# Kernel tuning notes

Measured on AMD Instinct MI355X. Metric: run time of the kernel, lower is better.

The kernel has to match this reference:

```python
import jax, jax.numpy as jnp
import numpy as np

THRESHOLDS = (0.3, 0.4, 0.5)
EPS_NORM = 1e-12   # F.normalize eps
EPS_MAX = 1e-5     # added to max before rescale


def setup_inputs() -> dict:
    key = jax.random.key(0)
    k1, k2 = jax.random.split(key)
    cam = jax.random.uniform(k1, (4, 64, 64), dtype=jnp.float32)
    feat = jax.random.normal(k2, (4, 256, 64, 64), dtype=jnp.float32)
    return {"cam": cam, "feat": feat}


def reference(cam, feat):
    # multi-threshold soft mask: mean of hard masks at each threshold -> (B,1,H,W)
    masks = jnp.stack([(cam >= t).astype(feat.dtype) for t in THRESHOLDS], axis=1)
    m = masks.mean(axis=1)[:, None]  # (B,1,H,W)
    masked = feat * m  # (B,C,H,W)

    B, C, H, W = masked.shape
    f = masked.reshape(B, C, H * W)  # (B,C,N)
    # L2-normalize over channel dim (torch F.normalize, dim=1)
    norm = jnp.sqrt(jnp.sum(f * f, axis=1, keepdims=True))
    fn = f / jnp.maximum(norm, EPS_NORM)

    # full pairwise similarity (B,N,N), then CAM-weighted aggregation
    sim = jnp.einsum('bcn,bcm->bnm', fn, fn)      # (B,N,N)
    camf = cam.reshape(B, H * W)                  # (B,N)
    out = jnp.einsum('bnm,bm->bn', sim, camf)     # (B,N)

    mn = out.min(axis=1, keepdims=True)
    mx = out.max(axis=1, keepdims=True) + EPS_MAX
    ref = ((out - mn) / (mx - mn)).reshape(B, H, W)

    loss = jnp.mean(jnp.abs(ref - jax.lax.stop_gradient(cam)))
    return ref, loss
```

## Files before the change

kernel.cpp:

```cpp
#include <hip/hip_runtime.h>


constexpr int B  = 4;
constexpr int C  = 256;
constexpr int N  = 4096;
constexpr int BN = B * N;
constexpr int CN = C * N;

__device__ __forceinline__ float wsum(float v) {
#pragma unroll
    for (int o = 32; o > 0; o >>= 1) v += __shfl_down(v, o, 64);
    return v;
}
__device__ __forceinline__ float wmin64(float v) {
#pragma unroll
    for (int o = 32; o > 0; o >>= 1) v = fminf(v, __shfl_down(v, o, 64));
    return v;
}
__device__ __forceinline__ float wmax64(float v) {
#pragma unroll
    for (int o = 32; o > 0; o >>= 1) v = fmaxf(v, __shfl_down(v, o, 64));
    return v;
}

__global__ void __launch_bounds__(256) k_norm(
    const float* __restrict__ cam, const float* __restrict__ feat,
    float* __restrict__ s, float* __restrict__ w, unsigned int* __restrict__ cnt)
{
    if (blockIdx.x == 0 && threadIdx.x == 0) *cnt = 0u;
    const int t   = threadIdx.x;
    const int pix = t & 31;
    const int g   = t >> 5;
    const int p   = blockIdx.x * 32 + pix;
    const int b   = p >> 12;
    const int n   = p & (N - 1);

    const float* fp = feat + (size_t)b * CN + (size_t)(g * 32) * N + n;
    float ss = 0.f;
#pragma unroll 8
    for (int cc = 0; cc < 32; ++cc) {
        float x = fp[(size_t)cc * N];
        ss = fmaf(x, x, ss);
    }
    __shared__ float red[8][33];
    red[g][pix] = ss;
    __syncthreads();
    if (t < 32) {
        float tot = 0.f;
#pragma unroll
        for (int gg = 0; gg < 8; ++gg) tot += red[gg][t];
        float cv = cam[blockIdx.x * 32 + t];
        float m  = ((cv >= 0.3f ? 1.f : 0.f) + (cv >= 0.4f ? 1.f : 0.f) +
                    (cv >= 0.5f ? 1.f : 0.f)) * (1.f / 3.f);
        tot *= m * m;
        float sc = m / fmaxf(sqrtf(tot), 1e-12f);
        int q = blockIdx.x * 32 + t;
        s[q] = sc;
        w[q] = sc * cv;
    }
}

__global__ void __launch_bounds__(256) k_v(
    const float* __restrict__ feat, const float* __restrict__ w,
    float* __restrict__ v)
{
    const int bc = blockIdx.x;
    const int b = bc >> 8, c = bc & (C - 1);
    const float* fp = feat + (size_t)b * CN + (size_t)c * N;
    const float* wp = w + b * N;
    const int t = threadIdx.x;
    float acc = 0.f;
#pragma unroll
    for (int i = 0; i < 4; ++i) {
        int idx = (i * 256 + t) * 4;
        float4 x = *(const float4*)(fp + idx);
        float4 y = *(const float4*)(wp + idx);
        acc = fmaf(x.x, y.x, acc); acc = fmaf(x.y, y.y, acc);
        acc = fmaf(x.z, y.z, acc); acc = fmaf(x.w, y.w, acc);
    }
    __shared__ float red[4];
    float tot = wsum(acc);
    if ((t & 63) == 0) red[t >> 6] = tot;
    __syncthreads();
    if (t == 0) v[bc] = (red[0] + red[1]) + (red[2] + red[3]);
}

__global__ void __launch_bounds__(256) k_out(
    const float* __restrict__ feat, const float* __restrict__ s,
    const float* __restrict__ v, float* __restrict__ ob,
    float* __restrict__ bmn, float* __restrict__ bmx)
{
    const int t   = threadIdx.x;
    const int pix = t & 31;
    const int g   = t >> 5;
    const int p   = blockIdx.x * 32 + pix;
    const int b   = p >> 12;
    const int n   = p & (N - 1);

    __shared__ float vs[C];
    vs[t] = v[b * C + t];
    __syncthreads();

    const float* fp = feat + (size_t)b * CN + (size_t)(g * 32) * N + n;
    float acc = 0.f;
#pragma unroll 8
    for (int cc = 0; cc < 32; ++cc)
        acc = fmaf(fp[(size_t)cc * N], vs[g * 32 + cc], acc);

    __shared__ float red[8][33];
    red[g][pix] = acc;
    __syncthreads();
    if (t < 32) {
        float tot = 0.f;
#pragma unroll
        for (int gg = 0; gg < 8; ++gg) tot += red[gg][t];
        float o = s[blockIdx.x * 32 + t] * tot;
        ob[blockIdx.x * 32 + t] = o;
        float mn = o, mx = o;
#pragma unroll
        for (int o2 = 16; o2 > 0; o2 >>= 1) {
            mn = fminf(mn, __shfl_down(mn, o2, 64));
            mx = fmaxf(mx, __shfl_down(mx, o2, 64));
        }
        if (t == 0) { bmn[blockIdx.x] = mn; bmx[blockIdx.x] = mx; }
    }
}

__global__ void __launch_bounds__(256) k_final(
    const float* __restrict__ ob, const float* __restrict__ cam,
    const float* __restrict__ bmn, const float* __restrict__ bmx,
    float* __restrict__ out, float* __restrict__ part, unsigned int* __restrict__ cnt)
{
    const int t = threadIdx.x, blk = blockIdx.x;
    const int p = blk * 256 + t;
    const int b = blk >> 4;

    __shared__ float sh[2];
    if (t < 64) {
        float a = fminf(bmn[b * 128 + t], bmn[b * 128 + 64 + t]);
        a = wmin64(a);
        if (t == 0) sh[0] = a;
    } else if (t < 128) {
        int l = t - 64;
        float a = fmaxf(bmx[b * 128 + l], bmx[b * 128 + 64 + l]);
        a = wmax64(a);
        if (l == 0) sh[1] = a;
    }
    __syncthreads();
    const float mn = sh[0];
    const float mx = sh[1] + 1e-5f;

    float r = (ob[p] - mn) / (mx - mn);
    out[p] = r;
    float ad = fabsf(r - cam[p]);

    __shared__ float red[4];
    float ps = wsum(ad);
    if ((t & 63) == 0) red[t >> 6] = ps;
    __syncthreads();

    __shared__ int lastflag;
    if (t == 0) {
        float tot = (red[0] + red[1]) + (red[2] + red[3]);
        __hip_atomic_store(&part[blk], tot, __ATOMIC_RELEASE, __HIP_MEMORY_SCOPE_AGENT);
        unsigned old = __hip_atomic_fetch_add(cnt, 1u, __ATOMIC_ACQ_REL,
                                              __HIP_MEMORY_SCOPE_AGENT);
        lastflag = (old == 63u) ? 1 : 0;
    }
    __syncthreads();
    if (lastflag && t < 64) {
        float x = __hip_atomic_load(&part[t], __ATOMIC_ACQUIRE,
                                    __HIP_MEMORY_SCOPE_AGENT);
        x = wsum(x);
        if (t == 0) out[BN] = x * (1.f / (float)BN);
    }
}

extern "C" void kernel_launch(void* const* d_in, const int* in_sizes, int n_in,
                              void* d_out, int out_size, void* d_ws, size_t ws_size,
                              hipStream_t stream) {
    const float* cam  = (const float*)d_in[0];
    const float* feat = (const float*)d_in[1];
    float* out = (float*)d_out;
    float* ws  = (float*)d_ws;

    float* s    = ws;
    float* w    = ws + 16384;
    float* v    = ws + 32768;
    float* ob   = ws + 33792;
    float* bmn  = ws + 50176;
    float* bmx  = ws + 50688;
    float* part = ws + 51200;
    unsigned int* cnt = (unsigned int*)(ws + 51264);

    k_norm <<<512,  256, 0, stream>>>(cam, feat, s, w, cnt);
    k_v    <<<1024, 256, 0, stream>>>(feat, w, v);
    k_out  <<<512,  256, 0, stream>>>(feat, s, v, ob, bmn, bmx);
    k_final<<<64,   256, 0, stream>>>(ob, cam, bmn, bmx, out, part, cnt);
}
```

Measured before the change: 20.37 us.

## Fuse channel-weighted reduction into norm kernel with partial sums and small reduce

Computes per-block partial sums of feat weighted by the normalized CAM weights inside the norm kernel, reusing the feature tile just loaded, instead of a separate kernel that re-reads all of feat. A small 4-block kernel then sums the 128 partials per batch into v. This removes one full pass over the feature tensor but adds a partial-sum buffer and a low-parallelism reduction kernel.

Measured after the change: 23.06 us. 13.2% more time.

```diff
diff --git a/kernel.cpp b/kernel.cpp
--- a/kernel.cpp
+++ b/kernel.cpp
@@ -6,6 +6,7 @@
 constexpr int N  = 4096;
 constexpr int BN = B * N;
 constexpr int CN = C * N;
+constexpr int NBLK1 = 512;
 
 __device__ __forceinline__ float wsum(float v) {
 #pragma unroll
@@ -23,66 +24,72 @@
     return v;
 }
 
-__global__ void __launch_bounds__(256) k_norm(
+__global__ void __launch_bounds__(256) k_norm_vpart(
     const float* __restrict__ cam, const float* __restrict__ feat,
-    float* __restrict__ s, float* __restrict__ w, unsigned int* __restrict__ cnt)
+    float* __restrict__ s, float* __restrict__ v_part,
+    unsigned int* __restrict__ cnt)
 {
     if (blockIdx.x == 0 && threadIdx.x == 0) *cnt = 0u;
     const int t   = threadIdx.x;
     const int pix = t & 31;
     const int g   = t >> 5;
-    const int p   = blockIdx.x * 32 + pix;
-    const int b   = p >> 12;
-    const int n   = p & (N - 1);
-
-    const float* fp = feat + (size_t)b * CN + (size_t)(g * 32) * N + n;
-    float ss = 0.f;
+    const int bk  = blockIdx.x;
+    const int b   = bk >> 7;
+    const int n0  = (bk * 32) & (N - 1);
+
+    __shared__ float red[8][33];
+    __shared__ float w_sh[32];
+
+    {
+        const float* fp = feat + (size_t)b * CN + (size_t)(g * 32) * N + n0 + pix;
+        float ss = 0.f;
 #pragma unroll 8
-    for (int cc = 0; cc < 32; ++cc) {
-        float x = fp[(size_t)cc * N];
-        ss = fmaf(x, x, ss);
-    }
-    __shared__ float red[8][33];
-    red[g][pix] = ss;
+        for (int cc = 0; cc < 32; ++cc) {
+            float x = fp[(size_t)cc * N];
+            ss = fmaf(x, x, ss);
+        }
+        red[g][pix] = ss;
+    }
     __syncthreads();
     if (t < 32) {
         float tot = 0.f;
 #pragma unroll
         for (int gg = 0; gg < 8; ++gg) tot += red[gg][t];
-        float cv = cam[blockIdx.x * 32 + t];
+        float cv = cam[bk * 32 + t];
         float m  = ((cv >= 0.3f ? 1.f : 0.f) + (cv >= 0.4f ? 1.f : 0.f) +
                     (cv >= 0.5f ? 1.f : 0.f)) * (1.f / 3.f);
-        tot *= m * m;
-        float sc = m / fmaxf(sqrtf(tot), 1e-12f);
-        int q = blockIdx.x * 32 + t;
-        s[q] = sc;
-        w[q] = sc * cv;
-    }
-}
-
-__global__ void __launch_bounds__(256) k_v(
-    const float* __restrict__ feat, const float* __restrict__ w,
-    float* __restrict__ v)
-{
-    const int bc = blockIdx.x;
-    const int b = bc >> 8, c = bc & (C - 1);
-    const float* fp = feat + (size_t)b * CN + (size_t)c * N;
-    const float* wp = w + b * N;
-    const int t = threadIdx.x;
+        float norm = m * sqrtf(tot);
+        float sc = m / fmaxf(norm, 1e-12f);
+        s[bk * 32 + t] = sc;
+        w_sh[t] = sc * cv;
+    }
+    __syncthreads();
+
+    {
+        const float* fp = feat + (size_t)b * CN + (size_t)t * N + n0;
+        float acc = 0.f;
+#pragma unroll
+        for (int pp = 0; pp < 8; ++pp) {
+            float4 x = *(const float4*)(fp + pp * 4);
+            acc = fmaf(x.x, w_sh[pp * 4 + 0], acc);
+            acc = fmaf(x.y, w_sh[pp * 4 + 1], acc);
+            acc = fmaf(x.z, w_sh[pp * 4 + 2], acc);
+            acc = fmaf(x.w, w_sh[pp * 4 + 3], acc);
+        }
+        v_part[bk * 256 + t] = acc;
+    }
+}
+
+__global__ void __launch_bounds__(256) k_vreduce(
+    const float* __restrict__ v_part, float* __restrict__ v)
+{
+    const int c = threadIdx.x;
+    const int b = blockIdx.x;
+    const float* base = v_part + (size_t)b * 128 * 256 + c;
     float acc = 0.f;
-#pragma unroll
-    for (int i = 0; i < 4; ++i) {
-        int idx = (i * 256 + t) * 4;
-        float4 x = *(const float4*)(fp + idx);
-        float4 y = *(const float4*)(wp + idx);
-        acc = fmaf(x.x, y.x, acc); acc = fmaf(x.y, y.y, acc);
-        acc = fmaf(x.z, y.z, acc); acc = fmaf(x.w, y.w, acc);
-    }
-    __shared__ float red[4];
-    float tot = wsum(acc);
-    if ((t & 63) == 0) red[t >> 6] = tot;
-    __syncthreads();
-    if (t == 0) v[bc] = (red[0] + red[1]) + (red[2] + red[3]);
+#pragma unroll 8
+    for (int k = 0; k < 128; ++k) acc += base[k * 256];
+    v[b * 256 + c] = acc;
 }
 
 __global__ void __launch_bounds__(256) k_out(
@@ -93,15 +100,15 @@
     const int t   = threadIdx.x;
     const int pix = t & 31;
     const int g   = t >> 5;
-    const int p   = blockIdx.x * 32 + pix;
-    const int b   = p >> 12;
-    const int n   = p & (N - 1);
+    const int bk  = blockIdx.x;
+    const int b   = bk >> 7;
+    const int n0  = (bk * 32) & (N - 1);
 
     __shared__ float vs[C];
     vs[t] = v[b * C + t];
     __syncthreads();
 
-    const float* fp = feat + (size_t)b * CN + (size_t)(g * 32) * N + n;
+    const float* fp = feat + (size_t)b * CN + (size_t)(g * 32) * N + n0 + pix;
     float acc = 0.f;
 #pragma unroll 8
     for (int cc = 0; cc < 32; ++cc)
@@ -114,15 +121,15 @@
         float tot = 0.f;
 #pragma unroll
         for (int gg = 0; gg < 8; ++gg) tot += red[gg][t];
-        float o = s[blockIdx.x * 32 + t] * tot;
-        ob[blockIdx.x * 32 + t] = o;
+        float o = s[bk * 32 + t] * tot;
+        ob[bk * 32 + t] = o;
         float mn = o, mx = o;
 #pragma unroll
         for (int o2 = 16; o2 > 0; o2 >>= 1) {
             mn = fminf(mn, __shfl_down(mn, o2, 64));
             mx = fmaxf(mx, __shfl_down(mx, o2, 64));
         }
-        if (t == 0) { bmn[blockIdx.x] = mn; bmx[blockIdx.x] = mx; }
+        if (t == 0) { bmn[bk] = mn; bmx[bk] = mx; }
     }
 }
 
@@ -184,17 +191,17 @@
     float* out = (float*)d_out;
     float* ws  = (float*)d_ws;
 
-    float* s    = ws;
-    float* w    = ws + 16384;
-    float* v    = ws + 32768;
-    float* ob   = ws + 33792;
-    float* bmn  = ws + 50176;
-    float* bmx  = ws + 50688;
-    float* part = ws + 51200;
-    unsigned int* cnt = (unsigned int*)(ws + 51264);
-
-    k_norm <<<512,  256, 0, stream>>>(cam, feat, s, w, cnt);
-    k_v    <<<1024, 256, 0, stream>>>(feat, w, v);
-    k_out  <<<512,  256, 0, stream>>>(feat, s, v, ob, bmn, bmx);
-    k_final<<<64,   256, 0, stream>>>(ob, cam, bmn, bmx, out, part, cnt);
-}
+    float* s      = ws;
+    float* v_part = ws + 16384;
+    float* v      = ws + 147456;
+    float* ob     = ws + 148480;
+    float* bmn    = ws + 164864;
+    float* bmx    = ws + 165376;
+    float* part   = ws + 165888;
+    unsigned int* cnt = (unsigned int*)(ws + 165952);
+
+    k_norm_vpart<<<NBLK1, 256, 0, stream>>>(cam, feat, s, v_part, cnt);
+    k_vreduce   <<<B,     256, 0, stream>>>(v_part, v);
+    k_out       <<<NBLK1, 256, 0, stream>>>(feat, s, v, ob, bmn, bmx);
+    k_final     <<<64,    256, 0, stream>>>(ob, cam, bmn, bmx, out, part, cnt);
+}
```
